# Kernel optimization log

Hardware: AMD Instinct MI355X
Metric: run time of the kernel (lower is better)

## Reference

```python
import math
import jax, jax.numpy as jnp
import numpy as np

HEAD = 16
DIM = 1024
DH = DIM // HEAD
NEG = -100000000.0


def setup_inputs() -> dict:
    key = jax.random.key(0)
    ks = jax.random.split(key, 12)
    B, S, D = 2, 2048, DIM
    s = 1.0 / math.sqrt(D)
    return {
        "key": jax.random.normal(ks[0], (B, S, D), jnp.float32),
        "value": jax.random.normal(ks[1], (B, S, D), jnp.float32),
        "query": jax.random.normal(ks[2], (B, S, D), jnp.float32),
        "mask": jax.random.randint(ks[3], (B, 1, S, S), 0, 2) == 1,
        "Wq": jax.random.normal(ks[4], (D, D), jnp.float32) * s,
        "bq": jnp.zeros((D,), jnp.float32),
        "Wk": jax.random.normal(ks[5], (D, D), jnp.float32) * s,
        "bk": jnp.zeros((D,), jnp.float32),
        "Wv": jax.random.normal(ks[6], (D, D), jnp.float32) * s,
        "bv": jnp.zeros((D,), jnp.float32),
        "Wo": jax.random.normal(ks[7], (D, D), jnp.float32) * s,
        "bo": jnp.zeros((D,), jnp.float32),
    }


def _split_heads(x, b):
    # [B, S, D] -> [B, H, S, Dh]
    return x.reshape(b, -1, HEAD, DH).transpose(0, 2, 1, 3)


def reference(key, value, query, mask, Wq, bq, Wk, bk, Wv, bv, Wo, bo):
    b, k_len, d = key.shape
    q_len = query.shape[1]
    k_up = _split_heads(key @ Wk.T + bk, b)
    v_up = _split_heads(value @ Wv.T + bv, b)
    q_up = _split_heads(query @ Wq.T + bq, b) / math.sqrt(DH)
    scores = jnp.einsum("bhqd,bhkd->bhqk", q_up, k_up)
    scores = jnp.where(mask, NEG, scores)
    attn = jax.nn.softmax(scores, axis=-1)
    # dropout is identity in eval/reference mode
    context = jnp.einsum("bhqk,bhkd->bhqd", attn, v_up)
    context = context.transpose(0, 2, 1, 3).reshape(b, q_len, d)
    out = context @ Wo.T + bo
    return out, attn
```

## Files before the change

### kernel.cpp

```cpp
#include <hip/hip_runtime.h>
#include <stdint.h>

#define S_LEN 2048
#define D_MODEL 1024
#define N_HEAD 16
#define D_HEAD 64
#define N_BATCH 2
#define M_TOK (N_BATCH * S_LEN)

typedef unsigned short u16;
typedef unsigned int u32;
typedef __attribute__((ext_vector_type(8))) short bf16x8;
typedef __attribute__((ext_vector_type(4))) float f32x4;
typedef __attribute__((ext_vector_type(4))) unsigned short u16x4;

#define MFMA16(a, b, c) __builtin_amdgcn_mfma_f32_16x16x32_bf16((a), (b), (c), 0, 0, 0)

__device__ __forceinline__ u16 f2bf(float f) {
  unsigned int u = __float_as_uint(f);
  u = (u + 0x7FFFu + ((u >> 16) & 1u)) >> 16;
  return (u16)u;
}

__device__ __forceinline__ void gload_lds16(const u16* g, u16* l) {
  __builtin_amdgcn_global_load_lds((const __attribute__((address_space(1))) void*)g,
                                   (__attribute__((address_space(3))) void*)l, 16, 0, 0);
}

#define N4BIG (M_TOK * D_MODEL / 4)
#define N4W (D_MODEL * D_MODEL / 4)
__global__ __launch_bounds__(256) void cvt7_kernel(
    const float* __restrict__ sk, const float* __restrict__ sv, const float* __restrict__ sq,
    const float* __restrict__ swq, const float* __restrict__ swk, const float* __restrict__ swv,
    const float* __restrict__ swo, u16* __restrict__ dk, u16* __restrict__ dv, u16* __restrict__ dq,
    u16* __restrict__ dwq, u16* __restrict__ dwk, u16* __restrict__ dwv, u16* __restrict__ dwo) {
  const float* s;
  u16* d;
  int n4;
  switch (blockIdx.y) {
    case 0: s = sk; d = dk; n4 = N4BIG; break;
    case 1: s = sv; d = dv; n4 = N4BIG; break;
    case 2: s = sq; d = dq; n4 = N4BIG; break;
    case 3: s = swq; d = dwq; n4 = N4W; break;
    case 4: s = swk; d = dwk; n4 = N4W; break;
    case 5: s = swv; d = dwv; n4 = N4W; break;
    default: s = swo; d = dwo; n4 = N4W; break;
  }
  int i = blockIdx.x * blockDim.x + threadIdx.x;
  int stride = gridDim.x * blockDim.x;
  for (; i < n4; i += stride) {
    float4 v = ((const float4*)s)[i];
    u16x4 o = {f2bf(v.x), f2bf(v.y), f2bf(v.z), f2bf(v.w)};
    ((u16x4*)d)[i] = o;
  }
}

__global__ __launch_bounds__(256) void pack_mask(const int* __restrict__ mask,
                                                 unsigned long long* __restrict__ packed) {
  int wid = (blockIdx.x * blockDim.x + threadIdx.x) >> 6;
  int lane = threadIdx.x & 63;
  int nw = (gridDim.x * blockDim.x) >> 6;
  const int NW64 = M_TOK * (S_LEN / 64);
  for (int widx = wid; widx < NW64; widx += nw) {
    int m = mask[(size_t)widx * 64 + lane];
    unsigned long long bits = __ballot(m != 0);
    if (lane == 0) packed[widx] = bits;
  }
}

__device__ __forceinline__ void gemm_body(const u16* __restrict__ A, const u16* __restrict__ Bw,
                                          const float* __restrict__ bias, void* __restrict__ Cout,
                                          float scale, int outmode) {
  __shared__ u16 As[128 * 32];
  __shared__ u16 Bs[128 * 32];
  const int K = D_MODEL, N = D_MODEL;
  int tid = threadIdx.x;
  int w = tid >> 6, lane = tid & 63, lg = lane >> 4, lr = lane & 15;
  int m0 = blockIdx.x * 128, n0 = blockIdx.y * 128;
  int wr = w >> 1, wc = w & 1;
  f32x4 acc[4][4] = {};
  int r0 = tid >> 2;
  int r1 = 64 + (tid >> 2);
  int kk0 = (tid & 3) * 8;
  for (int kb = 0; kb < K; kb += 32) {
    gload_lds16(A + (size_t)(m0 + r0) * K + kb + kk0, As + w * 512);
    gload_lds16(A + (size_t)(m0 + r1) * K + kb + kk0, As + 2048 + w * 512);
    gload_lds16(Bw + (size_t)(n0 + r0) * K + kb + kk0, Bs + w * 512);
    gload_lds16(Bw + (size_t)(n0 + r1) * K + kb + kk0, Bs + 2048 + w * 512);
    __syncthreads();
    bf16x8 af[4], bfr[4];
#pragma unroll
    for (int i = 0; i < 4; i++)
      af[i] = *(const bf16x8*)(As + (wr * 64 + i * 16 + lr) * 32 + lg * 8);
#pragma unroll
    for (int i = 0; i < 4; i++)
      bfr[i] = *(const bf16x8*)(Bs + (wc * 64 + i * 16 + lr) * 32 + lg * 8);
#pragma unroll
    for (int mi = 0; mi < 4; mi++)
#pragma unroll
      for (int ni = 0; ni < 4; ni++)
        acc[mi][ni] = MFMA16(af[mi], bfr[ni], acc[mi][ni]);
    __syncthreads();
  }
#pragma unroll
  for (int mi = 0; mi < 4; mi++)
#pragma unroll
    for (int ni = 0; ni < 4; ni++) {
      int col = n0 + wc * 64 + ni * 16 + lr;
      float bv = bias[col];
      if (outmode == 2) {
        int row0 = m0 + wr * 64 + mi * 16 + lg * 4;
        int bb = row0 >> 11, ss = row0 & (S_LEN - 1);
        u16x4 pk;
#pragma unroll
        for (int r = 0; r < 4; r++) pk[r] = f2bf((acc[mi][ni][r] + bv) * scale);
        *(u16x4*)((u16*)Cout + ((size_t)((bb * N_HEAD + (col >> 6)) * D_HEAD + (col & 63)) * S_LEN + ss)) = pk;
      } else {
#pragma unroll
        for (int r = 0; r < 4; r++) {
          int row = m0 + wr * 64 + mi * 16 + lg * 4 + r;
          float v = (acc[mi][ni][r] + bv) * scale;
          if (outmode == 1)
            ((float*)Cout)[(size_t)row * N + col] = v;
          else
            ((u16*)Cout)[(size_t)row * N + col] = f2bf(v);
        }
      }
    }
}

#define QSCALE 0.18033688011112042f

__global__ __launch_bounds__(256) void proj3_kernel(
    const u16* __restrict__ kbf, const u16* __restrict__ vbf, const u16* __restrict__ qbf,
    const u16* __restrict__ wkb, const u16* __restrict__ wvb, const u16* __restrict__ wqb,
    const float* __restrict__ bk, const float* __restrict__ bv, const float* __restrict__ bq,
    u16* __restrict__ kup, u16* __restrict__ vtg, u16* __restrict__ qup) {
  int z = blockIdx.z;
  if (z == 0)
    gemm_body(kbf, wkb, bk, kup, 1.0f, 0);
  else if (z == 1)
    gemm_body(vbf, wvb, bv, vtg, 1.0f, 2);
  else
    gemm_body(qbf, wqb, bq, qup, QSCALE, 0);
}

__global__ __launch_bounds__(256) void gemm_out_kernel(const u16* __restrict__ A,
                                                       const u16* __restrict__ Bw,
                                                       const float* __restrict__ bias,
                                                       float* __restrict__ C) {
  gemm_body(A, Bw, bias, C, 1.0f, 1);
}

__global__ __launch_bounds__(512, 4) void attn_kernel(
    const u16* __restrict__ Qup, const u16* __restrict__ Kup, const u16* __restrict__ Vt,
    const u32* __restrict__ mpack, float* __restrict__ attn_out, u16* __restrict__ ctx) {
  __shared__ u16 kbuf[2][64 * 64];
  __shared__ u16 vbuf[2][64 * 64];
  __shared__ u16 pbuf[8][16 * 64];
  int tid = threadIdx.x;
  int w = tid >> 6, lane = tid & 63, lg = lane >> 4, lr = lane & 15;
  int q0 = blockIdx.x * 128, h = blockIdx.y, b = blockIdx.z;
  int q = q0 + w * 16 + lr;
  const float NEGV = -100000000.0f;

  bf16x8 qf0, qf1;
  {
    const u16* qrow = Qup + (size_t)(b * S_LEN + q) * D_MODEL + h * D_HEAD;
    qf0 = *(const bf16x8*)(qrow + lg * 8);
    qf1 = *(const bf16x8*)(qrow + 32 + lg * 8);
  }
  const u16* Kb = Kup + (size_t)(b * S_LEN) * D_MODEL + h * D_HEAD;
  const u16* Vb = Vt + (size_t)(b * N_HEAD + h) * D_HEAD * S_LEN;
  const u32* mrow = mpack + (size_t)(b * S_LEN + q) * (S_LEN / 32);
  float* attn_b = attn_out + ((size_t)(b * N_HEAD + h) * S_LEN + q) * S_LEN;

  int srow = tid >> 3;
  int scs = (tid & 7) ^ (srow & 7);
  const u16* KgBase = Kb + (size_t)srow * D_MODEL + scs * 8;
  const u16* VgBase = Vb + (size_t)srow * S_LEN + scs * 8;
  const int sw = lr & 7;

  float lsum = 0.f;
  gload_lds16(KgBase, &kbuf[0][w * 512]);
  __syncthreads();
  for (int kt = 0; kt < 32; kt++) {
    int cur = kt & 1;
    if (kt < 31) gload_lds16(KgBase + (size_t)(kt + 1) * 64 * D_MODEL, &kbuf[cur ^ 1][w * 512]);
    const u16* kc = &kbuf[cur][0];
    uint2 mm = *(const uint2*)(mrow + kt * 2);
#pragma unroll
    for (int t = 0; t < 4; t++) {
      int rK = t * 16 + lr;
      bf16x8 k0 = *(const bf16x8*)(kc + rK * 64 + ((lg ^ sw) << 3));
      bf16x8 k1 = *(const bf16x8*)(kc + rK * 64 + (((lg + 4) ^ sw) << 3));
      f32x4 a = {0.f, 0.f, 0.f, 0.f};
      a = MFMA16(k0, qf0, a);
      a = MFMA16(k1, qf1, a);
      u32 wbits = (t < 2) ? mm.x : mm.y;
#pragma unroll
      for (int r = 0; r < 4; r++) {
        int j = (t * 16 + lg * 4 + r) & 31;
        float s = ((wbits >> j) & 1u) ? NEGV : a[r];
        lsum += exp2f(s);
      }
    }
    __syncthreads();
  }
  lsum += __shfl_xor(lsum, 16);
  lsum += __shfl_xor(lsum, 32);
  float inv_l = lsum > 0.f ? 1.0f / lsum : 0.f;

  f32x4 ctxacc[4] = {};
  u16* pw = &pbuf[w][0];
  gload_lds16(KgBase, &kbuf[0][w * 512]);
  gload_lds16(VgBase, &vbuf[0][w * 512]);
  __syncthreads();
  for (int kt = 0; kt < 32; kt++) {
    int cur = kt & 1;
    if (kt < 31) {
      gload_lds16(KgBase + (size_t)(kt + 1) * 64 * D_MODEL, &kbuf[cur ^ 1][w * 512]);
      gload_lds16(VgBase + (size_t)(kt + 1) * 64, &vbuf[cur ^ 1][w * 512]);
    }
    const u16* kc = &kbuf[cur][0];
    const u16* vc = &vbuf[cur][0];
    uint2 mm = *(const uint2*)(mrow + kt * 2);
    int kb = kt * 64;
#pragma unroll
    for (int t = 0; t < 4; t++) {
      int rK = t * 16 + lr;
      bf16x8 k0 = *(const bf16x8*)(kc + rK * 64 + ((lg ^ sw) << 3));
      bf16x8 k1 = *(const bf16x8*)(kc + rK * 64 + (((lg + 4) ^ sw) << 3));
      f32x4 a = {0.f, 0.f, 0.f, 0.f};
      a = MFMA16(k0, qf0, a);
      a = MFMA16(k1, qf1, a);
      u32 wbits = (t < 2) ? mm.x : mm.y;
      f32x4 p;
      u16x4 pb;
#pragma unroll
      for (int r = 0; r < 4; r++) {
        int j = (t * 16 + lg * 4 + r) & 31;
        float s = ((wbits >> j) & 1u) ? NEGV : a[r];
        float pv = exp2f(s) * inv_l;
        p[r] = pv;
        pb[r] = f2bf(pv);
      }
      *(f32x4*)(attn_b + kb + t * 16 + lg * 4) = p;
      *(u16x4*)(pw + lr * 64 + ((((t * 2) + (lg >> 1)) ^ sw) << 3) + ((lg & 1) << 2)) = pb;
    }
    bf16x8 pa0 = *(const bf16x8*)(pw + lr * 64 + ((lg ^ sw) << 3));
    bf16x8 pa1 = *(const bf16x8*)(pw + lr * 64 + (((lg + 4) ^ sw) << 3));
#pragma unroll
    for (int t = 0; t < 4; t++) {
      int rV = t * 16 + lr;
      bf16x8 v0 = *(const bf16x8*)(vc + rV * 64 + ((lg ^ sw) << 3));
      bf16x8 v1 = *(const bf16x8*)(vc + rV * 64 + (((lg + 4) ^ sw) << 3));
      ctxacc[t] = MFMA16(pa0, v0, ctxacc[t]);
      ctxacc[t] = MFMA16(pa1, v1, ctxacc[t]);
    }
    __syncthreads();
  }

#pragma unroll
  for (int t = 0; t < 4; t++)
#pragma unroll
    for (int r = 0; r < 4; r++) {
      int sq = q0 + w * 16 + lg * 4 + r;
      ctx[(size_t)(b * S_LEN + sq) * D_MODEL + h * D_HEAD + t * 16 + lr] = f2bf(ctxacc[t][r]);
    }
}

#define O_KBF 0u
#define O_VBF 4194304u
#define O_QBF 8388608u
#define O_WQ 12582912u
#define O_WK 13631488u
#define O_WV 14680064u
#define O_WO 15728640u
#define O_QUP 16777216u
#define O_KUP 20971520u
#define O_VUP 25165824u
#define O_CTX 29360128u

extern "C" void kernel_launch(void* const* d_in, const int* in_sizes, int n_in,
                              void* d_out, int out_size, void* d_ws, size_t ws_size,
                              hipStream_t stream) {
  const float* key = (const float*)d_in[0];
  const float* value = (const float*)d_in[1];
  const float* query = (const float*)d_in[2];
  const int* mask = (const int*)d_in[3];
  const float* Wq = (const float*)d_in[4];
  const float* bq = (const float*)d_in[5];
  const float* Wk = (const float*)d_in[6];
  const float* bk = (const float*)d_in[7];
  const float* Wv = (const float*)d_in[8];
  const float* bv = (const float*)d_in[9];
  const float* Wo = (const float*)d_in[10];
  const float* bo = (const float*)d_in[11];

  u16* ws = (u16*)d_ws;
  u16* kbf = ws + O_KBF;
  u16* vbf = ws + O_VBF;
  u16* qbf = ws + O_QBF;
  u16* wqb = ws + O_WQ;
  u16* wkb = ws + O_WK;
  u16* wvb = ws + O_WV;
  u16* wob = ws + O_WO;
  u16* qup = ws + O_QUP;
  u16* kup = ws + O_KUP;
  u16* vtg = ws + O_VUP;
  u16* ctxb = ws + O_CTX;

  float* out = (float*)d_out;
  float* attn = out + (size_t)N_BATCH * S_LEN * D_MODEL;

  cvt7_kernel<<<dim3(512, 7), 256, 0, stream>>>(key, value, query, Wq, Wk, Wv, Wo, kbf, vbf, qbf,
                                                wqb, wkb, wvb, wob);
  proj3_kernel<<<dim3(32, 8, 3), 256, 0, stream>>>(kbf, vbf, qbf, wkb, wvb, wqb, bk, bv, bq, kup,
                                                   vtg, qup);
  pack_mask<<<1024, 256, 0, stream>>>(mask, (unsigned long long*)kbf);
  attn_kernel<<<dim3(S_LEN / 128, N_HEAD, N_BATCH), 512, 0, stream>>>(qup, kup, vtg,
                                                                      (const u32*)kbf, attn, ctxb);
  gemm_out_kernel<<<dim3(32, 8), 256, 0, stream>>>(ctxb, wob, bo, out);
}
```

Before: 362.9 us.

## Feed P to PV MFMA from registers and remap attention blocks across XCDs

When the 16x16x16 bf16 MFMA builtin is available, the attention kernel passes the probability tile straight from registers as the A operand. This drops the per-wave LDS staging buffer and its write/read round trip. The price is twice as many smaller MFMAs and narrower V reads from LDS. The launch also becomes a flat 1D grid with an index remap that groups blocks sharing a (batch, head) onto the same XCD, so K/V loads get better L2 reuse.

```diff
diff --git a/kernel.cpp b/kernel.cpp
--- a/kernel.cpp
+++ b/kernel.cpp
@@ -11,10 +11,18 @@
 typedef unsigned short u16;
 typedef unsigned int u32;
 typedef __attribute__((ext_vector_type(8))) short bf16x8;
+typedef __attribute__((ext_vector_type(4))) short s16x4;
 typedef __attribute__((ext_vector_type(4))) float f32x4;
 typedef __attribute__((ext_vector_type(4))) unsigned short u16x4;
 
 #define MFMA16(a, b, c) __builtin_amdgcn_mfma_f32_16x16x32_bf16((a), (b), (c), 0, 0, 0)
+
+#if defined(__has_builtin)
+#if __has_builtin(__builtin_amdgcn_mfma_f32_16x16x16bf16_1k)
+#define HAVE_MFMA_16x16x16 1
+#define MFMA_PV(a, b, c) __builtin_amdgcn_mfma_f32_16x16x16bf16_1k((a), (b), (c), 0, 0, 0)
+#endif
+#endif
 
 __device__ __forceinline__ u16 f2bf(float f) {
   unsigned int u = __float_as_uint(f);
@@ -157,10 +165,18 @@
     const u32* __restrict__ mpack, float* __restrict__ attn_out, u16* __restrict__ ctx) {
   __shared__ u16 kbuf[2][64 * 64];
   __shared__ u16 vbuf[2][64 * 64];
+#if !defined(HAVE_MFMA_16x16x16)
   __shared__ u16 pbuf[8][16 * 64];
+#endif
   int tid = threadIdx.x;
   int w = tid >> 6, lane = tid & 63, lg = lane >> 4, lr = lane & 15;
-  int q0 = blockIdx.x * 128, h = blockIdx.y, b = blockIdx.z;
+
+  int fb = blockIdx.x;
+  int logical = (fb & 7) * 64 + (fb >> 3);
+  int qx = logical & 15;
+  int h = (logical >> 4) & 15;
+  int b = logical >> 8;
+  int q0 = qx * 128;
   int q = q0 + w * 16 + lr;
   const float NEGV = -100000000.0f;
 
@@ -212,7 +228,6 @@
   float inv_l = lsum > 0.f ? 1.0f / lsum : 0.f;
 
   f32x4 ctxacc[4] = {};
-  u16* pw = &pbuf[w][0];
   gload_lds16(KgBase, &kbuf[0][w * 512]);
   gload_lds16(VgBase, &vbuf[0][w * 512]);
   __syncthreads();
@@ -226,6 +241,9 @@
     const u16* vc = &vbuf[cur][0];
     uint2 mm = *(const uint2*)(mrow + kt * 2);
     int kb = kt * 64;
+#if defined(HAVE_MFMA_16x16x16)
+    s16x4 apv[4];
+#endif
 #pragma unroll
     for (int t = 0; t < 4; t++) {
       int rK = t * 16 + lr;
@@ -246,8 +264,25 @@
         pb[r] = f2bf(pv);
       }
       *(f32x4*)(attn_b + kb + t * 16 + lg * 4) = p;
-      *(u16x4*)(pw + lr * 64 + ((((t * 2) + (lg >> 1)) ^ sw) << 3) + ((lg & 1) << 2)) = pb;
-    }
+#if defined(HAVE_MFMA_16x16x16)
+      s16x4 ap = {(short)pb[0], (short)pb[1], (short)pb[2], (short)pb[3]};
+      apv[t] = ap;
+#else
+      *(u16x4*)(&pbuf[w][lr * 64 + ((((t * 2) + (lg >> 1)) ^ sw) << 3) + ((lg & 1) << 2)]) = pb;
+#endif
+    }
+#if defined(HAVE_MFMA_16x16x16)
+#pragma unroll
+    for (int t = 0; t < 4; t++) {
+#pragma unroll
+      for (int d = 0; d < 4; d++) {
+        s16x4 vf = *(const s16x4*)(vc + (d * 16 + lr) * 64 +
+                                   ((((t * 2) + (lg >> 1)) ^ sw) << 3) + ((lg & 1) << 2));
+        ctxacc[d] = MFMA_PV(apv[t], vf, ctxacc[d]);
+      }
+    }
+#else
+    u16* pw = &pbuf[w][0];
     bf16x8 pa0 = *(const bf16x8*)(pw + lr * 64 + ((lg ^ sw) << 3));
     bf16x8 pa1 = *(const bf16x8*)(pw + lr * 64 + (((lg + 4) ^ sw) << 3));
 #pragma unroll
@@ -258,6 +293,7 @@
       ctxacc[t] = MFMA16(pa0, v0, ctxacc[t]);
       ctxacc[t] = MFMA16(pa1, v1, ctxacc[t]);
     }
+#endif
     __syncthreads();
   }
 
@@ -319,7 +355,6 @@
   proj3_kernel<<<dim3(32, 8, 3), 256, 0, stream>>>(kbf, vbf, qbf, wkb, wvb, wqb, bk, bv, bq, kup,
                                                    vtg, qup);
   pack_mask<<<1024, 256, 0, stream>>>(mask, (unsigned long long*)kbf);
-  attn_kernel<<<dim3(S_LEN / 128, N_HEAD, N_BATCH), 512, 0, stream>>>(qup, kup, vtg,
-                                                                      (const u32*)kbf, attn, ctxb);
+  attn_kernel<<<512, 512, 0, stream>>>(qup, kup, vtg, (const u32*)kbf, attn, ctxb);
   gemm_out_kernel<<<dim3(32, 8), 256, 0, stream>>>(ctxb, wob, bo, out);
 }
```

Measured after the change: 354.8 us. -2.2%, faster.
